# Kernel optimization log

Hardware: AMD Instinct MI355X
Metric: run time of the kernel (lower is better)

The kernel has to match this reference:

```python
import jax, jax.numpy as jnp
import numpy as np

LMAX, MMAX = 6, 2
M_SIZE = (7, 6, 5)
SPHERE_C, HID = 128, 128
N_NODES, N_EDGES = 5000, 20000
N_COEFF_FULL = (LMAX + 1) ** 2                       # 49, l-primary node coeffs
N_COEFF_M = M_SIZE[0] + 2 * (M_SIZE[1] + M_SIZE[2])  # 29, m-primary edge coeffs
EXTRA_M0 = LMAX * HID                                # gate scalars from conv1


def _gate_idx():
    # maps each gated m-primary coefficient (all but l=0,m=0) to its degree index l-1
    idx = [l - 1 for l in range(1, LMAX + 1)]            # m=0 block (l=1..lmax)
    for m in range(1, MMAX + 1):
        for _ in range(2):                               # (-m, +m) components
            idx += [l - 1 for l in range(m, LMAX + 1)]
    return np.asarray(idx, dtype=np.int32)

GATE_IDX = jnp.asarray(_gate_idx())


def _layer_norm(h, s, b):
    mu = jnp.mean(h, axis=-1, keepdims=True)
    var = jnp.var(h, axis=-1, keepdims=True)
    return (h - mu) * jax.lax.rsqrt(var + 1e-5) * s + b


def _radial(e, w0, b0, s0, bb0, w1, b1, s1, bb1, w2, b2):
    h = jax.nn.silu(_layer_norm(e @ w0 + b0, s0, bb0))
    h = jax.nn.silu(_layer_norm(h @ w1 + b1, s1, bb1))
    return h @ w2 + b2


def _so2_conv(x, w_m0, b_m0, w_m1, w_m2, extra, x_rad=None):
    # x: [E, N_COEFF_M, C_in] in m-primary layout
    E = x.shape[0]
    w_m = (w_m1, w_m2)
    outs = []
    # m = 0: plain linear over flattened (l, channel)
    x0 = x[:, :M_SIZE[0]].reshape(E, -1)
    off_rad = 0
    if x_rad is not None:
        x0 = x0 * x_rad[:, :x0.shape[1]]
        off_rad = x0.shape[1]
    x0 = x0 @ w_m0 + b_m0
    x0_extra = None
    if extra:
        x0_extra, x0 = x0[:, :extra], x0[:, extra:]
    outs.append(x0.reshape(E, M_SIZE[0], -1))
    off = M_SIZE[0]
    # m > 0: complex-style SO(2) convolution per order m
    for m in range(1, MMAX + 1):
        sz = M_SIZE[m]
        xm = x[:, off:off + 2 * sz].reshape(E, 2, -1)    # [E, 2, sz*C_in]
        if x_rad is not None:
            d = xm.shape[2]
            xm = xm * x_rad[:, off_rad:off_rad + d][:, None, :]
            off_rad += d
        y = xm @ w_m[m - 1]                              # [E, 2, 2*sz*C_out]
        half = y.shape[2] // 2
        yr, yi = y[..., :half], y[..., half:]
        out_r = yr[:, 0] - yi[:, 1]
        out_i = yr[:, 1] + yi[:, 0]
        outs.append(jnp.stack((out_r, out_i), axis=1).reshape(E, 2 * sz, -1))
        off += 2 * sz
    out = jnp.concatenate(outs, axis=1)
    return (out, x0_extra) if extra else out


def _gate_act(gating, x):
    # gating: [E, LMAX*HID], x: [E, N_COEFF_M, HID]
    g = jax.nn.sigmoid(gating).reshape(-1, LMAX, HID)[:, GATE_IDX]  # [E, N_COEFF_M-1, HID]
    scalars = jax.nn.silu(x[:, :1])
    return jnp.concatenate((scalars, x[:, 1:] * g), axis=1)


def _edgewise(x, x_edge, edge_index, wig, wig_inv, env, params):
    (rw0, rb0, rs0, rbb0, rw1, rb1, rs1, rbb1, rw2, rb2,
     c1w0, c1b0, c1w1, c1w2, c2w0, c2b0, c2w1, c2w2) = params
    # gather source/target node features and concat channels -> [E, 49, 2C]
    msg = jnp.concatenate((x[edge_index[0]], x[edge_index[1]]), axis=2)
    # Wigner rotation + M mapping: l-primary (49) -> m-primary (29)
    msg = jnp.einsum('emj,ejc->emc', wig, msg)
    x_rad = _radial(x_edge, rw0, rb0, rs0, rbb0, rw1, rb1, rs1, rbb1, rw2, rb2)
    msg, gating = _so2_conv(msg, c1w0, c1b0, c1w1, c1w2, EXTRA_M0, x_rad)
    msg = _gate_act(gating, msg)
    msg = _so2_conv(msg, c2w0, c2b0, c2w1, c2w2, 0)
    msg = msg * env
    # inverse rotation: m-primary (29) -> l-primary (49)
    msg = jnp.einsum('ejm,emc->ejc', wig_inv, msg)
    return jax.ops.segment_sum(msg, edge_index[1], num_segments=x.shape[0])


def setup_inputs() -> dict:
    key = jax.random.key(0)
    ks = iter(jax.random.split(key, 40))
    def W(shape):
        return jax.random.normal(next(ks), shape, jnp.float32) / np.sqrt(shape[0])
    C_IN1 = 2 * SPHERE_C
    rad_out = C_IN1 * sum(M_SIZE)  # 4608
    inp = {}
    inp['x'] = jax.random.normal(next(ks), (N_NODES, N_COEFF_FULL, SPHERE_C), jnp.float32)
    inp['x_edge'] = jax.random.normal(next(ks), (N_EDGES, 128), jnp.float32)
    inp['edge_distance'] = jax.random.uniform(next(ks), (N_EDGES,), jnp.float32, 0.1, 6.0)
    inp['edge_index'] = jax.random.randint(next(ks), (2, N_EDGES), 0, N_NODES)
    inp['wigner_and_M_mapping'] = jax.random.normal(next(ks), (N_EDGES, N_COEFF_M, N_COEFF_FULL), jnp.float32) / np.sqrt(N_COEFF_FULL)
    inp['wigner_and_M_mapping_inv'] = jax.random.normal(next(ks), (N_EDGES, N_COEFF_FULL, N_COEFF_M), jnp.float32) / np.sqrt(N_COEFF_M)
    inp['edge_envelope'] = jax.random.uniform(next(ks), (N_EDGES, 1, 1), jnp.float32)
    inp['rad_w0'] = W((128, 256)); inp['rad_b0'] = jnp.zeros((256,), jnp.float32)
    inp['rad_ln0_s'] = jnp.ones((256,), jnp.float32); inp['rad_ln0_b'] = jnp.zeros((256,), jnp.float32)
    inp['rad_w1'] = W((256, 256)); inp['rad_b1'] = jnp.zeros((256,), jnp.float32)
    inp['rad_ln1_s'] = jnp.ones((256,), jnp.float32); inp['rad_ln1_b'] = jnp.zeros((256,), jnp.float32)
    inp['rad_w2'] = W((256, rad_out)); inp['rad_b2'] = jnp.zeros((rad_out,), jnp.float32)
    inp['c1_w_m0'] = W((M_SIZE[0] * C_IN1, M_SIZE[0] * HID + EXTRA_M0))
    inp['c1_b_m0'] = jnp.zeros((M_SIZE[0] * HID + EXTRA_M0,), jnp.float32)
    inp['c1_w_m1'] = W((M_SIZE[1] * C_IN1, 2 * M_SIZE[1] * HID))
    inp['c1_w_m2'] = W((M_SIZE[2] * C_IN1, 2 * M_SIZE[2] * HID))
    inp['c2_w_m0'] = W((M_SIZE[0] * HID, M_SIZE[0] * SPHERE_C))
    inp['c2_b_m0'] = jnp.zeros((M_SIZE[0] * SPHERE_C,), jnp.float32)
    inp['c2_w_m1'] = W((M_SIZE[1] * HID, 2 * M_SIZE[1] * SPHERE_C))
    inp['c2_w_m2'] = W((M_SIZE[2] * HID, 2 * M_SIZE[2] * SPHERE_C))
    return inp


def reference(x, x_edge, edge_distance, edge_index, wigner_and_M_mapping,
              wigner_and_M_mapping_inv, edge_envelope,
              rad_w0, rad_b0, rad_ln0_s, rad_ln0_b, rad_w1, rad_b1, rad_ln1_s, rad_ln1_b,
              rad_w2, rad_b2, c1_w_m0, c1_b_m0, c1_w_m1, c1_w_m2,
              c2_w_m0, c2_b_m0, c2_w_m1, c2_w_m2):
    # edge_distance is accepted (module signature) but unused in the original forward
    params = (rad_w0, rad_b0, rad_ln0_s, rad_ln0_b, rad_w1, rad_b1, rad_ln1_s, rad_ln1_b,
              rad_w2, rad_b2, c1_w_m0, c1_b_m0, c1_w_m1, c1_w_m2,
              c2_w_m0, c2_b_m0, c2_w_m1, c2_w_m2)
    return _edgewise(x, x_edge, edge_index, wigner_and_M_mapping,
                     wigner_and_M_mapping_inv, edge_envelope, params)
```

## Files before the change

kernel.cpp:

```cpp
#include <hip/hip_runtime.h>
#include <stdint.h>


#define E_NUM   20000
#define NN      5000

typedef uint16_t u16;
typedef __bf16  bf16x8 __attribute__((ext_vector_type(8)));
typedef float   f32x4  __attribute__((ext_vector_type(4)));
typedef uint16_t u16x8 __attribute__((ext_vector_type(8)));

__device__ __forceinline__ float bf2f(u16 h){
  uint32_t u = ((uint32_t)h) << 16;
  return __builtin_bit_cast(float, u);
}
__device__ __forceinline__ u16 f2bf(float f){
  uint32_t u = __builtin_bit_cast(uint32_t, f);
  u += 0x7fffu + ((u >> 16) & 1u);
  return (u16)(u >> 16);
}
__device__ __forceinline__ float sigm(float x){ return 1.f / (1.f + __expf(-x)); }

__device__ __forceinline__ void gload16(const void* g, void* l){
  __builtin_amdgcn_global_load_lds(
      (const __attribute__((address_space(1))) void*)g,
      (__attribute__((address_space(3))) void*)l, 16, 0, 0);
}

__device__ __forceinline__ int swz8(int orig, int nwg){
  int q = nwg >> 3, r = nwg & 7;
  int x = orig & 7, p = orig >> 3;
  int base = (x < r) ? x * (q + 1) : r * (q + 1) + (x - r) * q;
  return base + p;
}

__global__ void k_hist(const int* __restrict__ eidx, int* __restrict__ cnt){
  int e = blockIdx.x * 256 + threadIdx.x;
  if (e < E_NUM) atomicAdd(&cnt[eidx[E_NUM + e]], 1);
}
__global__ __launch_bounds__(256) void k_scan(const int* __restrict__ cnt,
                                              int* __restrict__ off){
  __shared__ int part[256];
  int t = threadIdx.x;
  int s = 0;
  #pragma unroll
  for (int i = 0; i < 20; ++i){
    int idx = t * 20 + i;
    if (idx < NN) s += cnt[idx];
  }
  part[t] = s;
  __syncthreads();
  if (t == 0){
    int run = 0;
    for (int i = 0; i < 256; ++i){ int v = part[i]; part[i] = run; run += v; }
  }
  __syncthreads();
  int run = part[t];
  #pragma unroll
  for (int i = 0; i < 20; ++i){
    int idx = t * 20 + i;
    if (idx < NN){ off[idx] = run; run += cnt[idx]; }
  }
}
__global__ void k_scatter(const int* __restrict__ eidx, int* __restrict__ off,
                          int* __restrict__ perm){
  int e = blockIdx.x * 256 + threadIdx.x;
  if (e < E_NUM){
    int pos = atomicAdd(&off[eidx[E_NUM + e]], 1);
    perm[pos] = e;
  }
}

__global__ void k_transpose_w(const float* __restrict__ in, u16* __restrict__ out,
                              int K, int N){
  __shared__ float t[32][33];
  int nb = blockIdx.x * 32, kb = blockIdx.y * 32;
  int tx = threadIdx.x & 31, ty = threadIdx.x >> 5;
  for (int i = ty; i < 32; i += 8)
    t[i][tx] = in[(size_t)(kb + i) * N + (nb + tx)];
  __syncthreads();
  for (int i = ty; i < 32; i += 8)
    out[(size_t)(nb + i) * K + (kb + tx)] = f2bf(t[tx][i]);
}

__global__ __launch_bounds__(256) void k_xpose(const float* __restrict__ x,
                                               u16* __restrict__ xT){
  __shared__ float t[6272];
  int n = blockIdx.x, tid = threadIdx.x;
  const float* xp = x + (size_t)n * 6272;
  for (int i = tid; i < 6272; i += 256) t[i] = xp[i];
  __syncthreads();
  int c = tid >> 1;
  int kh = (tid & 1) * 32;
  u16* o = xT + (size_t)n * 8192 + c * 64 + kh;
  #pragma unroll
  for (int q = 0; q < 4; ++q){
    u16x8 h;
    #pragma unroll
    for (int i = 0; i < 8; ++i){
      int k = kh + q * 8 + i;
      h[i] = (k < 49) ? f2bf(t[k * 128 + c]) : (u16)0;
    }
    *(u16x8*)(o + q * 8) = h;
  }
}

__global__ void k_gather_xe(const float* __restrict__ x_edge,
                            const int* __restrict__ perm,
                            u16* __restrict__ xe, int e0){
  int el = blockIdx.x, c = threadIdx.x;
  int pe = perm[e0 + el];
  xe[(size_t)el * 128 + c] = f2bf(x_edge[(size_t)pe * 128 + c]);
}

struct Seg {
  const u16* A; const u16* B; u16* C; const float* bias;
  int M, N, K, lda, blk0;
};
struct Seg5 { Seg s[5]; int nwg; };

__device__ __forceinline__ void gemm_tile(
    const u16* __restrict__ A, int lda, const u16* __restrict__ B,
    const float* __restrict__ bias, float* __restrict__ Cf,
    u16* __restrict__ Cb, int ldc, int M, int N, int K,
    int bm, int bn, u16* As , u16* Bs )
{
  const int tid  = threadIdx.x;
  const int lane = tid & 63;
  const int wave = tid >> 6;
  const int wm = wave >> 1, wn = wave & 1;
  const int fr = lane & 15, fq = lane >> 4;
  const int row0 = bm * 128;

  const int lr  = lane >> 2;
  const int lg  = lane & 3;
  const int rA0 = wave * 32 + lr;
  const int rA1 = rA0 + 16;
  const int g0  = lg ^ ((rA0 >> 1) & 3);
  const int g1  = lg ^ ((rA1 >> 1) & 3);
  int gra0 = row0 + rA0; if (gra0 > M - 1) gra0 = M - 1;
  int gra1 = row0 + rA1; if (gra1 > M - 1) gra1 = M - 1;
  const u16* aS0 = A + (size_t)gra0 * lda + g0 * 8;
  const u16* aS1 = A + (size_t)gra1 * lda + g1 * 8;
  const u16* bS0 = B + (size_t)(bn * 128 + rA0) * K + g0 * 8;
  const u16* bS1 = B + (size_t)(bn * 128 + rA1) * K + g1 * 8;
  const int dA0 = (wave * 32) * 32;
  const int dA1 = (wave * 32 + 16) * 32;

  int aoff[4], boff[4];
  #pragma unroll
  for (int mi = 0; mi < 4; ++mi){
    int r = wm * 64 + mi * 16 + fr;
    aoff[mi] = r * 32 + (fq ^ ((r >> 1) & 3)) * 8;
  }
  #pragma unroll
  for (int ni = 0; ni < 4; ++ni){
    int r = wn * 64 + ni * 16 + fr;
    boff[ni] = r * 32 + (fq ^ ((r >> 1) & 3)) * 8;
  }

  f32x4 acc[4][4];
  #pragma unroll
  for (int i = 0; i < 4; ++i)
    #pragma unroll
    for (int j = 0; j < 4; ++j) acc[i][j] = (f32x4){0.f, 0.f, 0.f, 0.f};

  auto stage = [&](int buf, int k0){
    gload16(aS0 + k0, &As[buf * 4096 + dA0]);
    gload16(aS1 + k0, &As[buf * 4096 + dA1]);
    gload16(bS0 + k0, &Bs[buf * 4096 + dA0]);
    gload16(bS1 + k0, &Bs[buf * 4096 + dA1]);
  };

  stage(0, 0);
  __syncthreads();
  int cur = 0;
  for (int k0 = 0; k0 < K; k0 += 32){
    if (k0 + 32 < K) stage(cur ^ 1, k0 + 32);
    bf16x8 af[4], bfv[4];
    #pragma unroll
    for (int mi = 0; mi < 4; ++mi)
      af[mi] = __builtin_bit_cast(bf16x8, *(const u16x8*)&As[cur * 4096 + aoff[mi]]);
    #pragma unroll
    for (int ni = 0; ni < 4; ++ni)
      bfv[ni] = __builtin_bit_cast(bf16x8, *(const u16x8*)&Bs[cur * 4096 + boff[ni]]);
    #pragma unroll
    for (int mi = 0; mi < 4; ++mi)
      #pragma unroll
      for (int ni = 0; ni < 4; ++ni)
        acc[mi][ni] = __builtin_amdgcn_mfma_f32_16x16x32_bf16(af[mi], bfv[ni], acc[mi][ni], 0, 0, 0);
    __syncthreads();
    cur ^= 1;
  }

  #pragma unroll
  for (int ni = 0; ni < 4; ++ni){
    int col = bn * 128 + wn * 64 + ni * 16 + fr;
    float bv = bias ? bias[col] : 0.f;
    #pragma unroll
    for (int mi = 0; mi < 4; ++mi){
      #pragma unroll
      for (int i = 0; i < 4; ++i){
        int row = row0 + wm * 64 + mi * 16 + fq * 4 + i;
        if (row < M){
          float v = acc[mi][ni][i] + bv;
          if (Cb) Cb[(size_t)row * ldc + col] = f2bf(v);
          else    Cf[(size_t)row * ldc + col] = v;
        }
      }
    }
  }
}

__global__ __launch_bounds__(256) void k_gemm_bt(
    const u16* __restrict__ A, int lda, const u16* __restrict__ B,
    const float* __restrict__ bias, float* __restrict__ Cf,
    u16* __restrict__ Cb, int ldc, int M, int N, int K)
{
  __shared__ u16 As[2 * 4096];
  __shared__ u16 Bs[2 * 4096];
  gemm_tile(A, lda, B, bias, Cf, Cb, ldc, M, N, K,
            blockIdx.y, blockIdx.x, As, Bs);
}

__global__ __launch_bounds__(256) void k_gemm_seg(Seg5 g)
{
  __shared__ u16 As[2 * 4096];
  __shared__ u16 Bs[2 * 4096];
  int wgid = swz8(blockIdx.x, g.nwg);
  Seg sg = g.s[4];
  if (wgid < g.s[4].blk0) sg = g.s[3];
  if (wgid < g.s[3].blk0) sg = g.s[2];
  if (wgid < g.s[2].blk0) sg = g.s[1];
  if (wgid < g.s[1].blk0) sg = g.s[0];
  int local = wgid - sg.blk0;
  int nbx = sg.N >> 7;
  int bn = local % nbx;
  int bm = local / nbx;
  gemm_tile(sg.A, sg.lda, sg.B, sg.bias, nullptr, sg.C, sg.N,
            sg.M, sg.N, sg.K, bm, bn, As, Bs);
}

__global__ __launch_bounds__(256) void k_ln_silu(
    const float* __restrict__ in, const float* __restrict__ sc,
    const float* __restrict__ bb, u16* __restrict__ out)
{
  int e = blockIdx.x, t = threadIdx.x;
  float v = in[(size_t)e * 256 + t];
  float s1 = v, s2 = v * v;
  #pragma unroll
  for (int off = 32; off > 0; off >>= 1){
    s1 += __shfl_down(s1, off);
    s2 += __shfl_down(s2, off);
  }
  __shared__ float r1[4], r2[4];
  if ((t & 63) == 0){ r1[t >> 6] = s1; r2[t >> 6] = s2; }
  __syncthreads();
  float S1 = r1[0] + r1[1] + r1[2] + r1[3];
  float S2 = r2[0] + r2[1] + r2[2] + r2[3];
  float mu  = S1 * (1.f / 256.f);
  float var = S2 * (1.f / 256.f) - mu * mu;
  float nv = (v - mu) * rsqrtf(var + 1e-5f) * sc[t] + bb[t];
  out[(size_t)e * 256 + t] = f2bf(nv * sigm(nv));
}

__global__ __launch_bounds__(256) void k_wig_fwd(
    const u16* __restrict__ xT, const int* __restrict__ eidx,
    const float* __restrict__ wig, const u16* __restrict__ xrad,
    u16* __restrict__ msgS, const int* __restrict__ perm, int e0)
{
  __shared__ u16 WL[32 * 64];
  int el = blockIdx.x, tid = threadIdx.x;
  int eg = perm[e0 + el];
  int lane = tid & 63, w = tid >> 6;

  const float* wp = wig + (size_t)eg * 1421;
  for (int idx = tid; idx < 2048; idx += 256){
    int m = idx >> 6, k = idx & 63;
    float v = (m < 29 && k < 49) ? wp[m * 49 + k] : 0.f;
    WL[m * 64 + ((((k >> 3) ^ (m & 7))) << 3) + (k & 7)] = f2bf(v);
  }

  const int fr = lane & 15, fq = lane >> 4;
  const int colbase = w * 64;
  int node = eidx[((w >> 1) ? E_NUM : 0) + eg];
  const u16* xb = xT + (size_t)node * 8192;
  bf16x8 bfv[4][2];
  #pragma unroll
  for (int ct = 0; ct < 4; ++ct)
    #pragma unroll
    for (int ks = 0; ks < 2; ++ks){
      int cc = ((w & 1) * 64) + ct * 16 + fr;
      bfv[ct][ks] = __builtin_bit_cast(bf16x8,
          *(const u16x8*)(xb + cc * 64 + (ks * 4 + fq) * 8));
    }
  __syncthreads();

  bf16x8 af[2][2];
  #pragma unroll
  for (int mt = 0; mt < 2; ++mt)
    #pragma unroll
    for (int ks = 0; ks < 2; ++ks){
      int m = mt * 16 + fr;
      int g = ks * 4 + fq;
      af[mt][ks] = __builtin_bit_cast(bf16x8,
          *(const u16x8*)&WL[m * 64 + ((g ^ (m & 7)) << 3)]);
    }
  f32x4 acc[2][4];
  #pragma unroll
  for (int mt = 0; mt < 2; ++mt)
    #pragma unroll
    for (int ct = 0; ct < 4; ++ct) acc[mt][ct] = (f32x4){0.f,0.f,0.f,0.f};
  #pragma unroll
  for (int mt = 0; mt < 2; ++mt)
    #pragma unroll
    for (int ct = 0; ct < 4; ++ct)
      #pragma unroll
      for (int ks = 0; ks < 2; ++ks)
        acc[mt][ct] = __builtin_amdgcn_mfma_f32_16x16x32_bf16(
            af[mt][ks], bfv[ct][ks], acc[mt][ct], 0, 0, 0);

  const u16* xr = xrad + (size_t)el * 4608;
  u16* o = msgS + (size_t)el * 7424;
  #pragma unroll
  for (int mt = 0; mt < 2; ++mt)
    #pragma unroll
    for (int ct = 0; ct < 4; ++ct){
      int col = colbase + ct * 16 + fr;
      #pragma unroll
      for (int r = 0; r < 4; ++r){
        int m = mt * 16 + fq * 4 + r;
        if (m < 29){
          int rr = (m < 13) ? m : (m < 24 ? m - 6 : m - 11);
          o[m * 256 + col] = f2bf(acc[mt][ct][r] * bf2f(xr[rr * 256 + col]));
        }
      }
    }
}

__global__ __launch_bounds__(128) void k_gate(
    const u16* __restrict__ c1m0, const u16* __restrict__ y10, const u16* __restrict__ y11,
    const u16* __restrict__ y20, const u16* __restrict__ y21, u16* __restrict__ msg2)
{
  int e = blockIdx.x, c = threadIdx.x;
  __shared__ float g[768];
  const u16* gp = c1m0 + (size_t)e * 1664;
  for (int i = c; i < 768; i += 128) g[i] = sigm(bf2f(gp[i]));
  __syncthreads();
  const u16* x0 = gp + 768;
  u16* o = msg2 + (size_t)e * 3712;
  { float v = bf2f(x0[c]); o[c] = f2bf(v * sigm(v)); }
  #pragma unroll
  for (int r = 1; r < 7; ++r)
    o[r * 128 + c] = f2bf(bf2f(x0[r * 128 + c]) * g[(r - 1) * 128 + c]);
  const u16* a0 = y10 + (size_t)e * 1536;
  const u16* a1 = y11 + (size_t)e * 1536;
  #pragma unroll
  for (int k = 0; k < 6; ++k){
    float orr = bf2f(a0[k * 128 + c]) - bf2f(a1[768 + k * 128 + c]);
    float oii = bf2f(a1[k * 128 + c]) + bf2f(a0[768 + k * 128 + c]);
    float gv = g[k * 128 + c];
    o[(7 + k)  * 128 + c] = f2bf(orr * gv);
    o[(13 + k) * 128 + c] = f2bf(oii * gv);
  }
  const u16* b0 = y20 + (size_t)e * 1280;
  const u16* b1 = y21 + (size_t)e * 1280;
  #pragma unroll
  for (int k = 0; k < 5; ++k){
    float orr = bf2f(b0[k * 128 + c]) - bf2f(b1[640 + k * 128 + c]);
    float oii = bf2f(b1[k * 128 + c]) + bf2f(b0[640 + k * 128 + c]);
    float gv = g[(1 + k) * 128 + c];
    o[(19 + k) * 128 + c] = f2bf(orr * gv);
    o[(24 + k) * 128 + c] = f2bf(oii * gv);
  }
}

__global__ __launch_bounds__(128) void k_recomb2(
    const u16* __restrict__ m3x0, const u16* __restrict__ z10, const u16* __restrict__ z11,
    const u16* __restrict__ z20, const u16* __restrict__ z21, const float* __restrict__ env,
    u16* __restrict__ msg3T, const int* __restrict__ perm, int e0)
{
  int e = blockIdx.x, c = threadIdx.x;
  float ev = env[perm[e0 + e]];
  u16 v[32];
  const u16* x0 = m3x0 + (size_t)e * 896;
  #pragma unroll
  for (int r = 0; r < 7; ++r) v[r] = f2bf(bf2f(x0[r * 128 + c]) * ev);
  const u16* a0 = z10 + (size_t)e * 1536;
  const u16* a1 = z11 + (size_t)e * 1536;
  #pragma unroll
  for (int k = 0; k < 6; ++k){
    float orr = bf2f(a0[k * 128 + c]) - bf2f(a1[768 + k * 128 + c]);
    float oii = bf2f(a1[k * 128 + c]) + bf2f(a0[768 + k * 128 + c]);
    v[7 + k]  = f2bf(orr * ev);
    v[13 + k] = f2bf(oii * ev);
  }
  const u16* b0 = z20 + (size_t)e * 1280;
  const u16* b1 = z21 + (size_t)e * 1280;
  #pragma unroll
  for (int k = 0; k < 5; ++k){
    float orr = bf2f(b0[k * 128 + c]) - bf2f(b1[640 + k * 128 + c]);
    float oii = bf2f(b1[k * 128 + c]) + bf2f(b0[640 + k * 128 + c]);
    v[19 + k] = f2bf(orr * ev);
    v[24 + k] = f2bf(oii * ev);
  }
  v[29] = 0; v[30] = 0; v[31] = 0;
  u16* o = msg3T + (size_t)e * 4096 + c * 32;
  #pragma unroll
  for (int q = 0; q < 4; ++q)
    *(u16x8*)(o + q * 8) = *(const u16x8*)(&v[q * 8]);
}

__global__ __launch_bounds__(256) void k_wig_inv(
    const u16* __restrict__ msg3T, const float* __restrict__ winv,
    const int* __restrict__ eidx, float* __restrict__ out,
    const int* __restrict__ perm, int e0, int cm)
{
  __shared__ u16 WV[64 * 32];
  int el = blockIdx.x, tid = threadIdx.x;
  int i = e0 + el;
  int d = eidx[E_NUM + perm[i]];
  if (el > 0 && eidx[E_NUM + perm[i - 1]] == d) return;
  int lane = tid & 63, w = tid >> 6;
  const int fr = lane & 15, fq = lane >> 4;
  const int jr = w * 16 + fr;

  f32x4 acc[8];
  #pragma unroll
  for (int ct = 0; ct < 8; ++ct) acc[ct] = (f32x4){0.f,0.f,0.f,0.f};

  int tend = e0 + cm;
  for (int t = i; t < tend; ++t){
    int pe = perm[t];
    if (t > i && eidx[E_NUM + pe] != d) break;
    __syncthreads();
    const float* wp = winv + (size_t)pe * 1421;
    for (int idx = tid; idx < 2048; idx += 256){
      int j = idx >> 5, m = idx & 31;
      float v = (j < 49 && m < 29) ? wp[j * 29 + m] : 0.f;
      WV[j * 32 + (((m >> 3) ^ (j & 3)) << 3) + (m & 7)] = f2bf(v);
    }
    __syncthreads();
    bf16x8 a = __builtin_bit_cast(bf16x8,
        *(const u16x8*)&WV[jr * 32 + ((fq ^ (jr & 3)) << 3)]);
    const u16* bp = msg3T + (size_t)(t - e0) * 4096;
    #pragma unroll
    for (int ct = 0; ct < 8; ++ct){
      bf16x8 b = __builtin_bit_cast(bf16x8,
          *(const u16x8*)(bp + (ct * 16 + fr) * 32 + fq * 8));
      acc[ct] = __builtin_amdgcn_mfma_f32_16x16x32_bf16(a, b, acc[ct], 0, 0, 0);
    }
  }

  float* op = out + (size_t)d * 6272;
  #pragma unroll
  for (int ct = 0; ct < 8; ++ct){
    int c = ct * 16 + fr;
    #pragma unroll
    for (int r = 0; r < 4; ++r){
      int j = w * 16 + fq * 4 + r;
      if (j < 49) atomicAdd(op + j * 128 + c, acc[ct][r]);
    }
  }
}

extern "C" void kernel_launch(void* const* d_in, const int* in_sizes, int n_in,
                              void* d_out, int out_size, void* d_ws, size_t ws_size,
                              hipStream_t stream)
{
  (void)in_sizes; (void)n_in;
  const float* x       = (const float*)d_in[0];
  const float* x_edge  = (const float*)d_in[1];
  const int*   eidx    = (const int*)d_in[3];
  const float* wig     = (const float*)d_in[4];
  const float* wig_inv = (const float*)d_in[5];
  const float* env     = (const float*)d_in[6];
  const float* rad_w0  = (const float*)d_in[7];
  const float* rad_b0  = (const float*)d_in[8];
  const float* ln0_s   = (const float*)d_in[9];
  const float* ln0_b   = (const float*)d_in[10];
  const float* rad_w1  = (const float*)d_in[11];
  const float* rad_b1  = (const float*)d_in[12];
  const float* ln1_s   = (const float*)d_in[13];
  const float* ln1_b   = (const float*)d_in[14];
  const float* rad_w2  = (const float*)d_in[15];
  const float* rad_b2  = (const float*)d_in[16];
  const float* c1w0    = (const float*)d_in[17];
  const float* c1b0    = (const float*)d_in[18];
  const float* c1w1    = (const float*)d_in[19];
  const float* c1w2    = (const float*)d_in[20];
  const float* c2w0    = (const float*)d_in[21];
  const float* c2b0    = (const float*)d_in[22];
  const float* c2w1    = (const float*)d_in[23];
  const float* c2w2    = (const float*)d_in[24];
  float* out = (float*)d_out;

  char* base = (char*)d_ws;
  size_t off = 0;
  auto alloc = [&](size_t bytes) -> char* {
    off = (off + 255) & ~(size_t)255;
    char* r = base + off;
    off += bytes;
    return r;
  };

  u16* wtR0  = (u16*)alloc((size_t)256  * 128  * 2);
  u16* wtR1  = (u16*)alloc((size_t)256  * 256  * 2);
  u16* wtR2  = (u16*)alloc((size_t)4608 * 256  * 2);
  u16* wtC10 = (u16*)alloc((size_t)1664 * 1792 * 2);
  u16* wtC11 = (u16*)alloc((size_t)1536 * 1536 * 2);
  u16* wtC12 = (u16*)alloc((size_t)1280 * 1280 * 2);
  u16* wtC20 = (u16*)alloc((size_t)896  * 896  * 2);
  u16* wtC21 = (u16*)alloc((size_t)1536 * 768  * 2);
  u16* wtC22 = (u16*)alloc((size_t)1280 * 640  * 2);
  u16* xT    = (u16*)alloc((size_t)NN * 8192 * 2);
  int* cnt   = (int*)alloc(NN * 4);
  int* soff  = (int*)alloc(NN * 4);
  int* perm  = (int*)alloc(E_NUM * 4);

  size_t fixed_end = (off + 65536) & ~(size_t)65535;
  size_t avail = (ws_size > fixed_end + (1u << 20)) ? (ws_size - fixed_end - (1u << 20)) : 0;
  long CH0 = (long)(avail / 40960);
  if (CH0 > E_NUM) CH0 = E_NUM;
  if (CH0 < 64) CH0 = 64;
  int nch = (int)((E_NUM + CH0 - 1) / CH0);
  int CH = (E_NUM + nch - 1) / nch;
  if (CH > CH0) CH = (int)CH0;

  off = fixed_end;
  const size_t C = (size_t)CH;
  u16*   xe   = (u16*)alloc(C * 128 * 2);
  float* tmp  = (float*)alloc(C * 256 * 4);
  u16*   h0   = (u16*)alloc(C * 256 * 2);
  u16*   h1   = (u16*)alloc(C * 256 * 2);
  u16* region1 = (u16*)alloc(C * 4608 * 2);
  u16* region2 = (u16*)alloc(C * 7424 * 2);
  u16* region3 = (u16*)alloc(C * 7296 * 2);
  u16* xrad = region1;
  u16* msg2 = region1;
  u16* msgS = region2;
  u16* m3x0 = region2;
  u16* z10  = region2 + C * 896;
  u16* z11  = region2 + C * 2432;
  u16* z20  = region2 + C * 3968;
  u16* z21  = region2 + C * 5248;
  u16* c1m0b = region3;
  u16* y10   = region3 + C * 1664;
  u16* y11   = region3 + C * 3200;
  u16* y20   = region3 + C * 4736;
  u16* y21   = region3 + C * 6016;
  u16* msg3T = region3;

  hipMemsetAsync(d_out, 0, (size_t)out_size * sizeof(float), stream);
  hipMemsetAsync(cnt, 0, NN * 4, stream);

  k_hist<<<(E_NUM + 255) / 256, 256, 0, stream>>>(eidx, cnt);
  k_scan<<<1, 256, 0, stream>>>(cnt, soff);
  k_scatter<<<(E_NUM + 255) / 256, 256, 0, stream>>>(eidx, soff, perm);
  k_xpose<<<NN, 256, 0, stream>>>(x, xT);

  auto tw = [&](const float* in, u16* o, int K, int N){
    k_transpose_w<<<dim3(N / 32, K / 32), 256, 0, stream>>>(in, o, K, N);
  };
  tw(rad_w0, wtR0, 128, 256);
  tw(rad_w1, wtR1, 256, 256);
  tw(rad_w2, wtR2, 256, 4608);
  tw(c1w0, wtC10, 1792, 1664);
  tw(c1w1, wtC11, 1536, 1536);
  tw(c1w2, wtC12, 1280, 1280);
  tw(c2w0, wtC20, 896, 896);
  tw(c2w1, wtC21, 768, 1536);
  tw(c2w2, wtC22, 640, 1280);

  auto gemm = [&](const u16* A, int lda, const u16* B, const float* bias,
                  float* Cf, u16* Cb, int ldc, int M, int N, int K){
    k_gemm_bt<<<dim3(N / 128, (M + 127) / 128), 256, 0, stream>>>(
        A, lda, B, bias, Cf, Cb, ldc, M, N, K);
  };

  for (int e0 = 0; e0 < E_NUM; e0 += CH){
    int cm = E_NUM - e0 < CH ? E_NUM - e0 : CH;
    int mb = (cm + 127) / 128;

    k_gather_xe<<<cm, 128, 0, stream>>>(x_edge, perm, xe, e0);

    gemm(xe, 128, wtR0, rad_b0, tmp, nullptr, 256, cm, 256, 128);
    k_ln_silu<<<cm, 256, 0, stream>>>(tmp, ln0_s, ln0_b, h0);
    gemm(h0, 256, wtR1, rad_b1, tmp, nullptr, 256, cm, 256, 256);
    k_ln_silu<<<cm, 256, 0, stream>>>(tmp, ln1_s, ln1_b, h1);
    gemm(h1, 256, wtR2, rad_b2, nullptr, xrad, 4608, cm, 4608, 256);

    k_wig_fwd<<<cm, 256, 0, stream>>>(xT, eidx, wig, xrad, msgS, perm, e0);

    {
      Seg5 g;
      int b = 0;
      auto mk = [&](const u16* A, const u16* B, u16* Cb, const float* bias,
                    int N, int K) -> Seg {
        Seg s{A, B, Cb, bias, cm, N, K, 7424, b};
        b += (N >> 7) * mb;
        return s;
      };
      g.s[0] = mk(msgS,        wtC10, c1m0b, c1b0,   1664, 1792);
      g.s[1] = mk(msgS + 1792, wtC11, y10,   nullptr, 1536, 1536);
      g.s[2] = mk(msgS + 3328, wtC11, y11,   nullptr, 1536, 1536);
      g.s[3] = mk(msgS + 4864, wtC12, y20,   nullptr, 1280, 1280);
      g.s[4] = mk(msgS + 6144, wtC12, y21,   nullptr, 1280, 1280);
      g.nwg = b;
      k_gemm_seg<<<b, 256, 0, stream>>>(g);
    }

    k_gate<<<cm, 128, 0, stream>>>(c1m0b, y10, y11, y20, y21, msg2);

    {
      Seg5 g;
      int b = 0;
      auto mk = [&](const u16* A, const u16* B, u16* Cb, const float* bias,
                    int N, int K) -> Seg {
        Seg s{A, B, Cb, bias, cm, N, K, 3712, b};
        b += (N >> 7) * mb;
        return s;
      };
      g.s[0] = mk(msg2,        wtC20, m3x0, c2b0,   896,  896);
      g.s[1] = mk(msg2 + 896,  wtC21, z10,  nullptr, 1536, 768);
      g.s[2] = mk(msg2 + 1664, wtC21, z11,  nullptr, 1536, 768);
      g.s[3] = mk(msg2 + 2432, wtC22, z20,  nullptr, 1280, 640);
      g.s[4] = mk(msg2 + 3072, wtC22, z21,  nullptr, 1280, 640);
      g.nwg = b;
      k_gemm_seg<<<b, 256, 0, stream>>>(g);
    }

    k_recomb2<<<cm, 128, 0, stream>>>(m3x0, z10, z11, z20, z21, env, msg3T, perm, e0);

    k_wig_inv<<<cm, 256, 0, stream>>>(msg3T, wig_inv, eidx, out, perm, e0, cm);
  }
}
```

Baseline: 2.438 ms.

## Deepen GEMM LDS pipeline to four stages with explicit vmcnt waits

The bf16 MFMA GEMM tile moves from double buffering to a four-stage LDS ring. Three K-slices are prefetched ahead, and explicit s_waitcnt vmcnt counts wait only for the slice about to be consumed. Bias loads are hoisted before the loop and drained once, so they do not disturb the vmcnt accounting. LDS use per block doubles to 64 KB, which may lower occupancy, and each iteration now has two barriers.

```diff
diff --git a/kernel.cpp b/kernel.cpp
--- a/kernel.cpp
+++ b/kernel.cpp
@@ -165,6 +165,16 @@
     #pragma unroll
     for (int j = 0; j < 4; ++j) acc[i][j] = (f32x4){0.f, 0.f, 0.f, 0.f};
 
+  float bv4[4];
+  #pragma unroll
+  for (int ni = 0; ni < 4; ++ni) bv4[ni] = 0.f;
+  if (bias){
+    #pragma unroll
+    for (int ni = 0; ni < 4; ++ni)
+      bv4[ni] = bias[bn * 128 + wn * 64 + ni * 16 + fr];
+  }
+  asm volatile("s_waitcnt vmcnt(0)" ::: "memory");
+
   auto stage = [&](int buf, int k0){
     gload16(aS0 + k0, &As[buf * 4096 + dA0]);
     gload16(aS1 + k0, &As[buf * 4096 + dA1]);
@@ -172,38 +182,51 @@
     gload16(bS1 + k0, &Bs[buf * 4096 + dA1]);
   };
 
+  const int nk = K >> 5;
   stage(0, 0);
-  __syncthreads();
-  int cur = 0;
-  for (int k0 = 0; k0 < K; k0 += 32){
-    if (k0 + 32 < K) stage(cur ^ 1, k0 + 32);
+  if (nk > 1) stage(1, 32);
+  if (nk > 2) stage(2, 64);
+  if (nk > 3) stage(3, 96);
+
+  for (int t = 0; t < nk; ++t){
+    int rem = nk - 1 - t;
+    if (rem >= 3)      asm volatile("s_waitcnt vmcnt(12)" ::: "memory");
+    else if (rem == 2) asm volatile("s_waitcnt vmcnt(8)"  ::: "memory");
+    else if (rem == 1) asm volatile("s_waitcnt vmcnt(4)"  ::: "memory");
+    else               asm volatile("s_waitcnt vmcnt(0)"  ::: "memory");
+    __builtin_amdgcn_s_barrier();
+    asm volatile("" ::: "memory");
+
+    const int cb = (t & 3) * 4096;
     bf16x8 af[4], bfv[4];
     #pragma unroll
     for (int mi = 0; mi < 4; ++mi)
-      af[mi] = __builtin_bit_cast(bf16x8, *(const u16x8*)&As[cur * 4096 + aoff[mi]]);
+      af[mi] = __builtin_bit_cast(bf16x8, *(const u16x8*)&As[cb + aoff[mi]]);
     #pragma unroll
     for (int ni = 0; ni < 4; ++ni)
-      bfv[ni] = __builtin_bit_cast(bf16x8, *(const u16x8*)&Bs[cur * 4096 + boff[ni]]);
+      bfv[ni] = __builtin_bit_cast(bf16x8, *(const u16x8*)&Bs[cb + boff[ni]]);
     #pragma unroll
     for (int mi = 0; mi < 4; ++mi)
       #pragma unroll
       for (int ni = 0; ni < 4; ++ni)
         acc[mi][ni] = __builtin_amdgcn_mfma_f32_16x16x32_bf16(af[mi], bfv[ni], acc[mi][ni], 0, 0, 0);
-    __syncthreads();
-    cur ^= 1;
+
+    asm volatile("" ::: "memory");
+    __builtin_amdgcn_s_barrier();
+    asm volatile("" ::: "memory");
+    if (t + 4 < nk) stage(t & 3, (t + 4) * 32);
   }
 
   #pragma unroll
   for (int ni = 0; ni < 4; ++ni){
     int col = bn * 128 + wn * 64 + ni * 16 + fr;
-    float bv = bias ? bias[col] : 0.f;
     #pragma unroll
     for (int mi = 0; mi < 4; ++mi){
       #pragma unroll
       for (int i = 0; i < 4; ++i){
         int row = row0 + wm * 64 + mi * 16 + fq * 4 + i;
         if (row < M){
-          float v = acc[mi][ni][i] + bv;
+          float v = acc[mi][ni][i] + bv4[ni];
           if (Cb) Cb[(size_t)row * ldc + col] = f2bf(v);
           else    Cf[(size_t)row * ldc + col] = v;
         }
@@ -217,16 +240,16 @@
     const float* __restrict__ bias, float* __restrict__ Cf,
     u16* __restrict__ Cb, int ldc, int M, int N, int K)
 {
-  __shared__ u16 As[2 * 4096];
-  __shared__ u16 Bs[2 * 4096];
+  __shared__ u16 As[4 * 4096];
+  __shared__ u16 Bs[4 * 4096];
   gemm_tile(A, lda, B, bias, Cf, Cb, ldc, M, N, K,
             blockIdx.y, blockIdx.x, As, Bs);
 }
 
 __global__ __launch_bounds__(256) void k_gemm_seg(Seg5 g)
 {
-  __shared__ u16 As[2 * 4096];
-  __shared__ u16 Bs[2 * 4096];
+  __shared__ u16 As[4 * 4096];
+  __shared__ u16 Bs[4 * 4096];
   int wgid = swz8(blockIdx.x, g.nwg);
   Seg sg = g.s[4];
   if (wgid < g.s[4].blk0) sg = g.s[3];
```

Result: slower. 2.608 ms (+7.0%).
